# Kernel optimization log

Measured on AMD Instinct MI355X. Metric: run time of the kernel, lower is better.

## Reference

```python
import jax, jax.numpy as jnp
import numpy as np

N_NODES = 100000
N_EDGES = 3200000
D_IN = 128
D_HID = 128


def setup_inputs() -> dict:
    key = jax.random.key(0)
    k1, k2, k3 = jax.random.split(key, 3)
    x = jax.random.normal(k1, (N_NODES, D_IN), dtype=jnp.float32)
    edge_index = jax.random.randint(k2, (2, N_EDGES), 0, N_NODES, dtype=jnp.int64)
    W = jax.random.normal(k3, (D_IN, D_HID), dtype=jnp.float32) * (1.0 / np.sqrt(D_IN))
    b = jnp.zeros((D_HID,), dtype=jnp.float32)
    return {"x": x, "edge_index": edge_index, "W": W, "b": b}


def reference(x, edge_index, W, b):
    N = x.shape[0]
    loop = jnp.arange(N, dtype=edge_index.dtype)
    src = jnp.concatenate([edge_index[0], loop])  # self-loops (PyG default)
    dst = jnp.concatenate([edge_index[1], loop])
    # symmetric normalization D^{-1/2} (A+I) D^{-1/2}
    deg = jax.ops.segment_sum(jnp.ones_like(src, dtype=x.dtype), dst, num_segments=N)
    dinv = jnp.where(deg > 0, jax.lax.rsqrt(deg), 0.0)
    norm = dinv[src] * dinv[dst]  # [E+N]
    h = x @ W  # [N, D_HID] transform before aggregation
    msg = h[src] * norm[:, None]  # gather + scale, [E+N, D_HID]
    agg = jax.ops.segment_sum(msg, dst, num_segments=N)  # scatter-add
    out = jax.nn.relu(agg + b)
    return out  # x_gmm branch is None (gmm not fitted)
```

## Files before the change

kernel.cpp:

```cpp
#include <hip/hip_runtime.h>

#define NN   100000
#define NE   3200000
#define D    128
#define NC   50
#define CSH  11
#define CCAP 67584
#define NF   3200
#define RCAP 1280
#define NSLICE 16
#define P2CAP (CCAP / NSLICE)
#define R1   4096

typedef __attribute__((ext_vector_type(8))) short short8v;
typedef __attribute__((ext_vector_type(4))) float f32x4;

__global__ void k_zero(int* __restrict__ cnt) {
    int i = blockIdx.x * 256 + threadIdx.x;
    if (i < NC + NF) cnt[i] = 0;
}

__global__ __launch_bounds__(256) void k_bin1(const int* __restrict__ src,
                                              const int* __restrict__ dst,
                                              int* __restrict__ gcnt,
                                              unsigned* __restrict__ creg) {
    __shared__ unsigned buf[R1], sorted[R1];
    __shared__ unsigned char bin8[R1], bsort[R1];
    __shared__ int hist[4 * NC], htot[NC], excl[NC], cur[4 * NC], gbase[NC];
    const int t = threadIdx.x, w = t >> 6;
    const int e0 = blockIdx.x * R1;
    const int n = min(R1, NE - e0);

    for (int i = t; i < 4 * NC; i += 256) hist[i] = 0;
    __syncthreads();
    for (int j = t; j < n; j += 256) {
        int d = dst[e0 + j], s = src[e0 + j];
        int b = d >> CSH;
        buf[j] = ((unsigned)(d & 2047) << 17) | (unsigned)s;
        bin8[j] = (unsigned char)b;
        atomicAdd(&hist[w * NC + b], 1);
    }
    __syncthreads();
    if (w == 0) {
        int b = t;
        int h0 = 0, h1 = 0, h2 = 0, h3 = 0, tot = 0;
        if (b < NC) {
            h0 = hist[b]; h1 = hist[NC + b]; h2 = hist[2 * NC + b]; h3 = hist[3 * NC + b];
            tot = h0 + h1 + h2 + h3;
        }
        int sc = tot;
        for (int off = 1; off < 64; off <<= 1) {
            int v = __shfl_up(sc, off, 64);
            if (t >= off) sc += v;
        }
        int ex = sc - tot;
        if (b < NC) {
            excl[b] = ex; htot[b] = tot;
            cur[b] = ex; cur[NC + b] = ex + h0;
            cur[2 * NC + b] = ex + h0 + h1; cur[3 * NC + b] = ex + h0 + h1 + h2;
        }
    }
    __syncthreads();
    for (int j = t; j < n; j += 256) {
        int b = bin8[j];
        int p = atomicAdd(&cur[w * NC + b], 1);
        sorted[p] = buf[j];
        bsort[p] = (unsigned char)b;
    }
    __syncthreads();
    if (t < NC) gbase[t] = htot[t] > 0 ? atomicAdd(&gcnt[t], htot[t]) : 0;
    __syncthreads();
    for (int j = t; j < n; j += 256) {
        int b = bsort[j];
        int p = gbase[b] + (j - excl[b]);
        if (p < CCAP) creg[(size_t)b * CCAP + p] = sorted[j];
    }
}

__global__ __launch_bounds__(256) void k_bin2(const int* __restrict__ gcnt,
                                              const unsigned* __restrict__ creg,
                                              int* __restrict__ fcnt,
                                              unsigned* __restrict__ freg) {
    __shared__ unsigned buf[P2CAP], sorted[P2CAP];
    __shared__ unsigned char bin8[P2CAP], bsort[P2CAP];
    __shared__ int hist[4 * 64], htot[64], excl[64], cur[4 * 64], gbase[64];
    const int t = threadIdx.x, w = t >> 6;
    const int c = blockIdx.x >> 4;
    const int sl = blockIdx.x & (NSLICE - 1);
    const int cnt = min(gcnt[c], CCAP);
    const int slice = (cnt + NSLICE - 1) / NSLICE;
    const int j0 = sl * slice;
    const int n = max(0, min(slice, cnt - j0));
    const unsigned* reg = creg + (size_t)c * CCAP + j0;

    for (int i = t; i < 4 * 64; i += 256) hist[i] = 0;
    __syncthreads();
    for (int j = t; j < n; j += 256) {
        unsigned v = reg[j];
        int b = (v >> 22) & 63;
        buf[j] = v;
        bin8[j] = (unsigned char)b;
        atomicAdd(&hist[w * 64 + b], 1);
    }
    __syncthreads();
    if (w == 0) {
        int b = t;
        int h0 = hist[b], h1 = hist[64 + b], h2 = hist[128 + b], h3 = hist[192 + b];
        int tot = h0 + h1 + h2 + h3;
        int sc = tot;
        for (int off = 1; off < 64; off <<= 1) {
            int v = __shfl_up(sc, off, 64);
            if (t >= off) sc += v;
        }
        int ex = sc - tot;
        excl[b] = ex; htot[b] = tot;
        cur[b] = ex; cur[64 + b] = ex + h0;
        cur[128 + b] = ex + h0 + h1; cur[192 + b] = ex + h0 + h1 + h2;
    }
    __syncthreads();
    for (int j = t; j < n; j += 256) {
        int b = bin8[j];
        int p = atomicAdd(&cur[w * 64 + b], 1);
        sorted[p] = buf[j];
        bsort[p] = (unsigned char)b;
    }
    __syncthreads();
    if (t < 64) gbase[t] = htot[t] > 0 ? atomicAdd(&fcnt[c * 64 + t], htot[t]) : 0;
    __syncthreads();
    for (int j = t; j < n; j += 256) {
        int b = bsort[j];
        int p = gbase[b] + (j - excl[b]);
        if (p < RCAP) freg[(size_t)(c * 64 + b) * RCAP + p] = sorted[j];
    }
}

__global__ __launch_bounds__(256) void k_sort(const int* __restrict__ fcnt,
                                              unsigned* __restrict__ freg,
                                              uint2* __restrict__ offs,
                                              float* __restrict__ dinv) {
    __shared__ unsigned buf[RCAP], sorted[RCAP];
    __shared__ int hist[32], cur[32], hexcl[32];
    const int f = blockIdx.x, t = threadIdx.x;
    if (f * 32 >= NN) return;
    const int n = min(fcnt[f], RCAP);
    unsigned* reg = freg + (size_t)f * RCAP;

    if (t < 32) hist[t] = 0;
    __syncthreads();
    for (int j = t; j < n; j += 256) {
        unsigned v = reg[j];
        buf[j] = v;
        atomicAdd(&hist[(v >> 17) & 31], 1);
    }
    __syncthreads();
    if (t == 0) {
        int a = 0;
        for (int i = 0; i < 32; ++i) { hexcl[i] = a; cur[i] = a; a += hist[i]; }
    }
    __syncthreads();
    for (int j = t; j < n; j += 256) {
        unsigned v = buf[j];
        int p = atomicAdd(&cur[(v >> 17) & 31], 1);
        sorted[p] = v;
    }
    __syncthreads();
    for (int j = t; j < n; j += 256) reg[j] = sorted[j];
    if (t < 32) {
        int node = f * 32 + t;
        if (node < NN) {
            offs[node] = make_uint2((unsigned)(f * RCAP + hexcl[t]), (unsigned)hist[t]);
            dinv[node] = rsqrtf(1.0f + (float)hist[t]);
        }
    }
}

__device__ __forceinline__ unsigned bf16_rne(float f) {
    unsigned u = __float_as_uint(f);
    u += 0x7fffu + ((u >> 16) & 1u);
    return u >> 16;
}

#define SWZ(row, kb) (((((row) << 8) | ((kb) << 1))) ^ ((((row) & 7)) << 4))

__global__ __launch_bounds__(256) void k_gemm(const float* __restrict__ x,
                                              const float* __restrict__ W,
                                              const float* __restrict__ dinv,
                                              unsigned* __restrict__ h2, int nrows) {
    __shared__ short xs[128 * 128];
    __shared__ short wt[128 * 128];
    const int t = threadIdx.x;
    const int row0 = blockIdx.x * 128;

    {
        const int n = t & 127, kh = (t >> 7) * 64;
        for (int j = 0; j < 8; ++j) {
            int k0 = kh + j * 8;
            short8v pk;
#pragma unroll
            for (int e = 0; e < 8; ++e)
                pk[e] = (short)bf16_rne(W[(k0 + e) * 128 + n]);
            *(short8v*)&wt[SWZ(n, k0) >> 1] = pk;
        }
    }
    for (int p = 0; p < 8; ++p) {
        int idx = p * 256 + t;
        int r = idx >> 4, k8 = (idx & 15) * 8;
        int row = row0 + r;
        short8v pk = {0, 0, 0, 0, 0, 0, 0, 0};
        if (row < nrows) {
            float4 v0 = *(const float4*)&x[(size_t)row * D + k8];
            float4 v1 = *(const float4*)&x[(size_t)row * D + k8 + 4];
            pk[0] = (short)bf16_rne(v0.x); pk[1] = (short)bf16_rne(v0.y);
            pk[2] = (short)bf16_rne(v0.z); pk[3] = (short)bf16_rne(v0.w);
            pk[4] = (short)bf16_rne(v1.x); pk[5] = (short)bf16_rne(v1.y);
            pk[6] = (short)bf16_rne(v1.z); pk[7] = (short)bf16_rne(v1.w);
        }
        *(short8v*)&xs[SWZ(r, k8) >> 1] = pk;
    }
    __syncthreads();

    const int w = t >> 6, l = t & 63;
    const int lr = l & 15, lg = l >> 4;

    f32x4 acc[2][8];
#pragma unroll
    for (int i = 0; i < 2; ++i)
#pragma unroll
        for (int j = 0; j < 8; ++j)
            acc[i][j] = (f32x4){0.f, 0.f, 0.f, 0.f};

#pragma unroll
    for (int ks = 0; ks < 4; ++ks) {
        const int kb = ks * 32 + lg * 8;
        short8v a0 = *(const short8v*)&xs[SWZ(w * 32 + lr, kb) >> 1];
        short8v a1 = *(const short8v*)&xs[SWZ(w * 32 + 16 + lr, kb) >> 1];
#pragma unroll
        for (int nt = 0; nt < 8; ++nt) {
            short8v bv = *(const short8v*)&wt[SWZ(nt * 16 + lr, kb) >> 1];
            acc[0][nt] = __builtin_amdgcn_mfma_f32_16x16x32_bf16(a0, bv, acc[0][nt], 0, 0, 0);
            acc[1][nt] = __builtin_amdgcn_mfma_f32_16x16x32_bf16(a1, bv, acc[1][nt], 0, 0, 0);
        }
    }

#pragma unroll
    for (int rt = 0; rt < 2; ++rt) {
#pragma unroll
        for (int rg = 0; rg < 4; ++rg) {
            int row = row0 + w * 32 + rt * 16 + lg * 4 + rg;
            float di = (row < nrows) ? dinv[row] : 0.f;
#pragma unroll
            for (int nt = 0; nt < 8; ++nt) {
                unsigned u = bf16_rne(acc[rt][nt][rg] * di);
                unsigned o = (unsigned)__shfl_xor((int)u, 1);
                if (!(lr & 1) && row < nrows)
                    h2[(size_t)row * 64 + nt * 8 + (lr >> 1)] = u | (o << 16);
            }
        }
    }
}

__device__ __forceinline__ float lo_f(unsigned v) { return __uint_as_float(v << 16); }
__device__ __forceinline__ float hi_f(unsigned v) { return __uint_as_float(v & 0xffff0000u); }

__global__ __launch_bounds__(256) void k_agg(const unsigned* __restrict__ h2,
                                             const float* __restrict__ dinv,
                                             const uint2* __restrict__ offs,
                                             const unsigned* __restrict__ region,
                                             const float* __restrict__ bias,
                                             float* __restrict__ out) {
    const int wave = threadIdx.x >> 6;
    const int lane = threadIdx.x & 63;
    const int node = blockIdx.x * 4 + wave;
    if (node >= NN) return;
    const int g = lane >> 4;
    const int q = lane & 15;

    const uint2 o = offs[node];
    const unsigned* reg = region + o.x;
    const int n = (int)o.y;

    float acc[8] = {0.f, 0.f, 0.f, 0.f, 0.f, 0.f, 0.f, 0.f};

#define ADD8(V) do { \
        acc[0] += lo_f((V).x); acc[1] += hi_f((V).x); \
        acc[2] += lo_f((V).y); acc[3] += hi_f((V).y); \
        acc[4] += lo_f((V).z); acc[5] += hi_f((V).z); \
        acc[6] += lo_f((V).w); acc[7] += hi_f((V).w); } while (0)

    if (g == 0) {
        uint4 v = *(const uint4*)&h2[(size_t)node * 64 + q * 4];
        ADD8(v);
    }

    int base = 0;
    for (; base + 8 <= n; base += 8) {
        int s0 = reg[base + g]     & 0x1FFFF;
        int s1 = reg[base + 4 + g] & 0x1FFFF;
        uint4 v0 = *(const uint4*)&h2[(size_t)s0 * 64 + q * 4];
        uint4 v1 = *(const uint4*)&h2[(size_t)s1 * 64 + q * 4];
        ADD8(v0);
        ADD8(v1);
    }
    for (; base < n; base += 4) {
        int e = base + g;
        if (e < n) {
            int s = reg[e] & 0x1FFFF;
            uint4 v = *(const uint4*)&h2[(size_t)s * 64 + q * 4];
            ADD8(v);
        }
    }
#undef ADD8

#pragma unroll
    for (int i = 0; i < 8; ++i) {
        acc[i] += __shfl_xor(acc[i], 16);
        acc[i] += __shfl_xor(acc[i], 32);
    }

    const float di = dinv[node];
    const int c = q * 8 + g * 2;
    float2 bb = *(const float2*)&bias[c];
    float2 r;
    r.x = fmaxf(di * acc[g * 2]     + bb.x, 0.f);
    r.y = fmaxf(di * acc[g * 2 + 1] + bb.y, 0.f);
    *(float2*)&out[(size_t)node * D + c] = r;
}

extern "C" void kernel_launch(void* const* d_in, const int* in_sizes, int n_in,
                              void* d_out, int out_size, void* d_ws, size_t ws_size,
                              hipStream_t stream) {
    const float* x  = (const float*)d_in[0];
    const int*   ei = (const int*)d_in[1];
    const float* W  = (const float*)d_in[2];
    const float* b  = (const float*)d_in[3];
    float* out = (float*)d_out;

    unsigned* h2   = (unsigned*)d_ws;
    float*    dinv = (float*)(h2 + (size_t)NN * 64);
    uint2*    offs = (uint2*)(dinv + NN);
    int*      gcnt = (int*)(offs + NN);
    int*      fcnt = gcnt + NC;
    unsigned* creg = (unsigned*)(fcnt + NF);
    unsigned* freg = creg + (size_t)NC * CCAP;

    const int* src = ei;
    const int* dst = ei + NE;

    k_zero<<<(NC + NF + 255) / 256, 256, 0, stream>>>(gcnt);
    k_bin1<<<(NE + R1 - 1) / R1, 256, 0, stream>>>(src, dst, gcnt, creg);
    k_bin2<<<NC * NSLICE, 256, 0, stream>>>(gcnt, creg, fcnt, freg);
    k_sort<<<NF, 256, 0, stream>>>(fcnt, freg, offs, dinv);
    k_gemm<<<(NN + 127) / 128, 256, 0, stream>>>(x, W, dinv, h2, NN);
    k_agg <<<(NN + 3) / 4, 256, 0, stream>>>(h2, dinv, offs, freg, b, out);
}
```

Baseline: 201.6 us.

## Fuse per-bucket counting sort into aggregation kernel, sort by dst then src bucket

```diff
diff --git a/kernel.cpp b/kernel.cpp
--- a/kernel.cpp
+++ b/kernel.cpp
@@ -134,43 +134,22 @@
     }
 }
 
-__global__ __launch_bounds__(256) void k_sort(const int* __restrict__ fcnt,
-                                              unsigned* __restrict__ freg,
-                                              uint2* __restrict__ offs,
-                                              float* __restrict__ dinv) {
-    __shared__ unsigned buf[RCAP], sorted[RCAP];
-    __shared__ int hist[32], cur[32], hexcl[32];
+__global__ __launch_bounds__(256) void k_deg(const int* __restrict__ fcnt,
+                                             const unsigned* __restrict__ freg,
+                                             float* __restrict__ dinv) {
+    __shared__ int hist[32];
     const int f = blockIdx.x, t = threadIdx.x;
     if (f * 32 >= NN) return;
+    if (t < 32) hist[t] = 0;
+    __syncthreads();
     const int n = min(fcnt[f], RCAP);
-    unsigned* reg = freg + (size_t)f * RCAP;
-
-    if (t < 32) hist[t] = 0;
-    __syncthreads();
-    for (int j = t; j < n; j += 256) {
-        unsigned v = reg[j];
-        buf[j] = v;
-        atomicAdd(&hist[(v >> 17) & 31], 1);
-    }
-    __syncthreads();
-    if (t == 0) {
-        int a = 0;
-        for (int i = 0; i < 32; ++i) { hexcl[i] = a; cur[i] = a; a += hist[i]; }
-    }
-    __syncthreads();
-    for (int j = t; j < n; j += 256) {
-        unsigned v = buf[j];
-        int p = atomicAdd(&cur[(v >> 17) & 31], 1);
-        sorted[p] = v;
-    }
-    __syncthreads();
-    for (int j = t; j < n; j += 256) reg[j] = sorted[j];
+    const unsigned* reg = freg + (size_t)f * RCAP;
+    for (int j = t; j < n; j += 256)
+        atomicAdd(&hist[(reg[j] >> 17) & 31], 1);
+    __syncthreads();
     if (t < 32) {
         int node = f * 32 + t;
-        if (node < NN) {
-            offs[node] = make_uint2((unsigned)(f * RCAP + hexcl[t]), (unsigned)hist[t]);
-            dinv[node] = rsqrtf(1.0f + (float)hist[t]);
-        }
+        if (node < NN) dinv[node] = rsqrtf(1.0f + (float)hist[t]);
     }
 }
 
@@ -264,22 +243,55 @@
 
 __global__ __launch_bounds__(256) void k_agg(const unsigned* __restrict__ h2,
                                              const float* __restrict__ dinv,
-                                             const uint2* __restrict__ offs,
-                                             const unsigned* __restrict__ region,
+                                             const int* __restrict__ fcnt,
+                                             const unsigned* __restrict__ freg,
                                              const float* __restrict__ bias,
                                              float* __restrict__ out) {
-    const int wave = threadIdx.x >> 6;
-    const int lane = threadIdx.x & 63;
-    const int node = blockIdx.x * 4 + wave;
-    if (node >= NN) return;
+    __shared__ unsigned buf[RCAP], sorted[RCAP];
+    __shared__ int hist[256], cur[256], excl[257];
+    const int f = blockIdx.x, t = threadIdx.x;
+    const int node0 = f * 32;
+    if (node0 >= NN) return;
+    const int n = min(fcnt[f], RCAP);
+    const unsigned* reg = freg + (size_t)f * RCAP;
+
+    hist[t] = 0;
+    __syncthreads();
+    for (int j = t; j < n; j += 256) {
+        unsigned v = reg[j];
+        buf[j] = v;
+        int key = (int)(((v >> 17) & 31u) * 8u + ((v >> 14) & 7u));
+        atomicAdd(&hist[key], 1);
+    }
+    __syncthreads();
+    if (t < 64) {
+        int h0 = hist[t * 4], h1 = hist[t * 4 + 1];
+        int h2v = hist[t * 4 + 2], h3 = hist[t * 4 + 3];
+        int s = h0 + h1 + h2v + h3;
+        int sc = s;
+        for (int off = 1; off < 64; off <<= 1) {
+            int v = __shfl_up(sc, off, 64);
+            if (t >= off) sc += v;
+        }
+        int base = sc - s;
+        excl[t * 4] = base;                cur[t * 4] = base;
+        excl[t * 4 + 1] = base + h0;       cur[t * 4 + 1] = base + h0;
+        excl[t * 4 + 2] = base + h0 + h1;  cur[t * 4 + 2] = base + h0 + h1;
+        excl[t * 4 + 3] = base + h0 + h1 + h2v; cur[t * 4 + 3] = base + h0 + h1 + h2v;
+        if (t == 63) excl[256] = sc;
+    }
+    __syncthreads();
+    for (int j = t; j < n; j += 256) {
+        unsigned v = buf[j];
+        int key = (int)(((v >> 17) & 31u) * 8u + ((v >> 14) & 7u));
+        int p = atomicAdd(&cur[key], 1);
+        sorted[p] = v;
+    }
+    __syncthreads();
+
+    const int w = t >> 6, lane = t & 63;
     const int g = lane >> 4;
     const int q = lane & 15;
-
-    const uint2 o = offs[node];
-    const unsigned* reg = region + o.x;
-    const int n = (int)o.y;
-
-    float acc[8] = {0.f, 0.f, 0.f, 0.f, 0.f, 0.f, 0.f, 0.f};
 
 #define ADD8(V) do { \
         acc[0] += lo_f((V).x); acc[1] += hi_f((V).x); \
@@ -287,43 +299,49 @@
         acc[4] += lo_f((V).z); acc[5] += hi_f((V).z); \
         acc[6] += lo_f((V).w); acc[7] += hi_f((V).w); } while (0)
 
-    if (g == 0) {
-        uint4 v = *(const uint4*)&h2[(size_t)node * 64 + q * 4];
-        ADD8(v);
-    }
-
-    int base = 0;
-    for (; base + 8 <= n; base += 8) {
-        int s0 = reg[base + g]     & 0x1FFFF;
-        int s1 = reg[base + 4 + g] & 0x1FFFF;
-        uint4 v0 = *(const uint4*)&h2[(size_t)s0 * 64 + q * 4];
-        uint4 v1 = *(const uint4*)&h2[(size_t)s1 * 64 + q * 4];
-        ADD8(v0);
-        ADD8(v1);
-    }
-    for (; base < n; base += 4) {
-        int e = base + g;
-        if (e < n) {
-            int s = reg[e] & 0x1FFFF;
-            uint4 v = *(const uint4*)&h2[(size_t)s * 64 + q * 4];
+    for (int i = 0; i < 8; ++i) {
+        const int dl = w * 8 + i;
+        const int node = node0 + dl;
+        if (node >= NN) break;
+        const int start = excl[dl * 8];
+        const int end = excl[(dl + 1) * 8];
+
+        float acc[8] = {0.f, 0.f, 0.f, 0.f, 0.f, 0.f, 0.f, 0.f};
+        if (g == 0) {
+            uint4 v = *(const uint4*)&h2[(size_t)node * 64 + q * 4];
             ADD8(v);
         }
+        int base = start;
+        for (; base + 8 <= end; base += 8) {
+            int s0 = (int)(sorted[base + g]     & 0x1FFFFu);
+            int s1 = (int)(sorted[base + 4 + g] & 0x1FFFFu);
+            uint4 v0 = *(const uint4*)&h2[(size_t)s0 * 64 + q * 4];
+            uint4 v1 = *(const uint4*)&h2[(size_t)s1 * 64 + q * 4];
+            ADD8(v0);
+            ADD8(v1);
+        }
+        for (; base < end; base += 4) {
+            int e = base + g;
+            if (e < end) {
+                int s = (int)(sorted[e] & 0x1FFFFu);
+                uint4 v = *(const uint4*)&h2[(size_t)s * 64 + q * 4];
+                ADD8(v);
+            }
+        }
+#pragma unroll
+        for (int k = 0; k < 8; ++k) {
+            acc[k] += __shfl_xor(acc[k], 16);
+            acc[k] += __shfl_xor(acc[k], 32);
+        }
+        const float di = dinv[node];
+        const int c = q * 8 + g * 2;
+        float2 bb = *(const float2*)&bias[c];
+        float2 r;
+        r.x = fmaxf(di * acc[g * 2]     + bb.x, 0.f);
+        r.y = fmaxf(di * acc[g * 2 + 1] + bb.y, 0.f);
+        *(float2*)&out[(size_t)node * D + c] = r;
     }
 #undef ADD8
-
-#pragma unroll
-    for (int i = 0; i < 8; ++i) {
-        acc[i] += __shfl_xor(acc[i], 16);
-        acc[i] += __shfl_xor(acc[i], 32);
-    }
-
-    const float di = dinv[node];
-    const int c = q * 8 + g * 2;
-    float2 bb = *(const float2*)&bias[c];
-    float2 r;
-    r.x = fmaxf(di * acc[g * 2]     + bb.x, 0.f);
-    r.y = fmaxf(di * acc[g * 2 + 1] + bb.y, 0.f);
-    *(float2*)&out[(size_t)node * D + c] = r;
 }
 
 extern "C" void kernel_launch(void* const* d_in, const int* in_sizes, int n_in,
@@ -337,8 +355,7 @@
 
     unsigned* h2   = (unsigned*)d_ws;
     float*    dinv = (float*)(h2 + (size_t)NN * 64);
-    uint2*    offs = (uint2*)(dinv + NN);
-    int*      gcnt = (int*)(offs + NN);
+    int*      gcnt = (int*)(dinv + NN);
     int*      fcnt = gcnt + NC;
     unsigned* creg = (unsigned*)(fcnt + NF);
     unsigned* freg = creg + (size_t)NC * CCAP;
@@ -349,7 +366,7 @@
     k_zero<<<(NC + NF + 255) / 256, 256, 0, stream>>>(gcnt);
     k_bin1<<<(NE + R1 - 1) / R1, 256, 0, stream>>>(src, dst, gcnt, creg);
     k_bin2<<<NC * NSLICE, 256, 0, stream>>>(gcnt, creg, fcnt, freg);
-    k_sort<<<NF, 256, 0, stream>>>(fcnt, freg, offs, dinv);
+    k_deg <<<NF, 256, 0, stream>>>(fcnt, freg, dinv);
     k_gemm<<<(NN + 127) / 128, 256, 0, stream>>>(x, W, dinv, h2, NN);
-    k_agg <<<(NN + 3) / 4, 256, 0, stream>>>(h2, dinv, offs, freg, b, out);
-}
+    k_agg <<<NF, 256, 0, stream>>>(h2, dinv, fcnt, freg, b, out);
+}
```

Result: no change. 199.0 us (median of 2 runs) (-1.3%).
